# Kernel tuning notes

Hardware: AMD Instinct MI355X
Metric: run time of the kernel (lower is better)

Reference implementation:

```python
import jax, jax.numpy as jnp
import numpy as np

N = 100000   # nodes
E = 1600000  # edges (avg degree 16)
D = 128      # in_dim


def setup_inputs() -> dict:
    key = jax.random.key(0)
    k = jax.random.split(key, 8)
    h = jax.random.normal(k[0], (N, D), dtype=jnp.float32)
    d = jax.random.uniform(k[1], (N,), dtype=jnp.float32)  # per-node degree norm (e.g. deg^-0.5)
    yes_no = jax.random.uniform(k[2], (E,), dtype=jnp.float32)
    gate_w = jax.random.normal(k[3], (1, 2 * D), dtype=jnp.float32) * (1.414 / np.sqrt(2 * D))
    gate_b = jnp.zeros((1,), dtype=jnp.float32)
    yes_weight = jax.random.uniform(k[4], (), dtype=jnp.float32)
    no_weight = jax.random.uniform(k[5], (), dtype=jnp.float32)
    src = jax.random.randint(k[6], (E,), 0, N, dtype=jnp.int64)
    dst = jax.random.randint(k[7], (E,), 0, N, dtype=jnp.int64)
    return {"h": h, "d": d, "yes_no": yes_no, "gate_w": gate_w, "gate_b": gate_b,
            "yes_weight": yes_weight, "no_weight": no_weight, "src": src, "dst": dst}


def reference(h, d, yes_no, gate_w, gate_b, yes_weight, no_weight, src, dst):
    n, dim = h.shape
    # gate(cat[h_dst, h_src]) == h_dst @ W[:, :D].T + h_src @ W[:, D:].T + b
    # project once per node, then gather per edge (avoids [E, 2D] concat)
    p_dst = h @ gate_w[0, :dim]  # [N]
    p_src = h @ gate_w[0, dim:]  # [N]
    g = jnp.tanh(p_dst[dst] + p_src[src] + gate_b[0])  # [E]
    yn = jnp.tanh(yes_no * yes_weight + (1.0 - yes_no) * no_weight)  # [E]
    e = (g + yn) * 0.5 * d[dst] * d[src]  # [E] (dropout p=0 -> identity)
    m = h[src] * e[:, None]  # [E, D] edge messages
    z = jax.ops.segment_sum(m, dst, num_segments=n)  # [N, D]
    return z
```

## Files before the change

kernel.cpp:

```cpp
#include <hip/hip_runtime.h>

#define D 128
#define NPB 250
#define NBMAX 512
#define EPB 2048
#define BCAP 5120

typedef unsigned short u16x8 __attribute__((ext_vector_type(8)));
typedef float          f32x8 __attribute__((ext_vector_type(8)));
typedef float          f32x4 __attribute__((ext_vector_type(4)));

__device__ __forceinline__ unsigned short f2bf(float x) {
    unsigned int u = __float_as_uint(x);
    u += 0x7FFFu + ((u >> 16) & 1u);
    return (unsigned short)(u >> 16);
}
__device__ __forceinline__ float bf2f(unsigned short b) {
    return __uint_as_float(((unsigned int)b) << 16);
}
__device__ __forceinline__ float fast_tanh(float x) {
    float e = __expf(2.0f * x);
    return 1.0f - 2.0f * __builtin_amdgcn_rcpf(e + 1.0f);
}

__global__ __launch_bounds__(256) void proj_kernel(const float* __restrict__ h,
                                                   const float* __restrict__ gw,
                                                   const float* __restrict__ dnorm,
                                                   float4* __restrict__ q,
                                                   unsigned short* __restrict__ hb,
                                                   unsigned int* __restrict__ tails,
                                                   int n_nodes) {
    if (blockIdx.x == 0) {
        tails[threadIdx.x] = 0u;
        tails[threadIdx.x + 256] = 0u;
    }
    int node = (int)((blockIdx.x * blockDim.x + threadIdx.x) >> 6);
    int lane = threadIdx.x & 63;
    if (node >= n_nodes) return;
    const float2* hr2 = (const float2*)(h + (size_t)node * D);
    const float2* gw2 = (const float2*)gw;
    float2 hv = hr2[lane];
    float2 wa = gw2[lane];
    float2 wb = gw2[lane + 64];
    ushort2 hvb = make_ushort2(f2bf(hv.x), f2bf(hv.y));
    *(ushort2*)(hb + (size_t)node * D + 2 * lane) = hvb;
    float s1 = hv.x * wa.x + hv.y * wa.y;
    float s2 = hv.x * wb.x + hv.y * wb.y;
    #pragma unroll
    for (int off = 32; off > 0; off >>= 1) {
        s1 += __shfl_down(s1, off, 64);
        s2 += __shfl_down(s2, off, 64);
    }
    if (lane == 0) q[node] = make_float4(s1, s2, dnorm[node], 0.0f);
}

__global__ __launch_bounds__(512) void bin_kernel(const float4* __restrict__ q,
                                                  const float* __restrict__ yes_no,
                                                  const int* __restrict__ src,
                                                  const int* __restrict__ dst,
                                                  const float* __restrict__ gate_b,
                                                  const float* __restrict__ yes_w,
                                                  const float* __restrict__ no_w,
                                                  unsigned int* __restrict__ tails,
                                                  unsigned long long* __restrict__ recs,
                                                  int n_edges, int nb) {
    __shared__ unsigned long long sorted[EPB];
    __shared__ unsigned int hist[NBMAX];
    __shared__ unsigned int sbuf[NBMAX];
    __shared__ unsigned int base[NBMAX];
    __shared__ unsigned int cursor[NBMAX];
    __shared__ unsigned int gbase[NBMAX];

    int tid = threadIdx.x;
    int e0 = blockIdx.x * EPB;
    int n = n_edges - e0;
    if (n > EPB) n = EPB;

    hist[tid] = 0u;
    __syncthreads();

    for (int j = tid; j < n; j += 512) {
        unsigned int d = (unsigned int)dst[e0 + j];
        atomicAdd(&hist[d / NPB], 1u);
    }
    __syncthreads();

    sbuf[tid] = hist[tid];
    __syncthreads();
    unsigned int* pa = sbuf;
    unsigned int* pb = gbase;
    #pragma unroll
    for (int s = 1; s < NBMAX; s <<= 1) {
        unsigned int v = pa[tid] + ((tid >= s) ? pa[tid - s] : 0u);
        pb[tid] = v;
        __syncthreads();
        unsigned int* t = pa; pa = pb; pb = t;
    }
    unsigned int ex = (tid == 0) ? 0u : pa[tid - 1];
    base[tid] = ex;
    cursor[tid] = ex;
    __syncthreads();

    float gb = gate_b[0];
    float yw = yes_w[0];
    float nw = no_w[0];

    for (int j = tid; j < n; j += 512) {
        int e = e0 + j;
        int dd = dst[e];
        int ss = src[e];
        float yn = yes_no[e];
        float4 qt = q[dd];
        float4 qs = q[ss];
        float g = fast_tanh(qt.x + qs.y + gb);
        float y = fast_tanh(yn * yw + (1.0f - yn) * nw);
        float ce = (g + y) * 0.5f * qt.z * qs.z;
        int qv = (int)rintf(ce * 8191.0f) + 8192;
        unsigned int w0 = ((unsigned int)ss << 15) | (unsigned int)qv;
        unsigned int bk = (unsigned int)dd / NPB;
        unsigned int pos = atomicAdd(&cursor[bk], 1u);
        sorted[pos] = ((unsigned long long)(unsigned int)dd << 32) | (unsigned long long)w0;
    }
    __syncthreads();

    gbase[tid] = (hist[tid] > 0u) ? atomicAdd(&tails[tid], hist[tid]) : 0u;
    __syncthreads();

    for (int j = tid; j < n; j += 512) {
        unsigned long long r = sorted[j];
        unsigned int bk = (unsigned int)(r >> 32) / NPB;
        unsigned int gpos = gbase[bk] + ((unsigned int)j - base[bk]);
        if (gpos < BCAP)
            __builtin_nontemporal_store(r, recs + (size_t)bk * BCAP + gpos);
    }
}

__global__ __launch_bounds__(512) void gscat_kernel(const unsigned int* __restrict__ tails,
                                                    const unsigned long long* __restrict__ recs,
                                                    const unsigned short* __restrict__ hb,
                                                    float* __restrict__ z,
                                                    int n_nodes) {
    __shared__ unsigned int sw0[BCAP];
    __shared__ unsigned int hist2[256];
    __shared__ unsigned int sa[256];
    __shared__ unsigned int sb[256];
    __shared__ unsigned int rowbase[256];
    __shared__ unsigned int cursor2[256];

    int b = blockIdx.x;
    int tid = threadIdx.x;
    unsigned int nrec = tails[b];
    if (nrec > BCAP) nrec = BCAP;
    const unsigned long long* rb = recs + (size_t)b * BCAP;
    int node0 = b * NPB;

    if (tid < 256) hist2[tid] = 0u;
    __syncthreads();

    for (unsigned int j = tid; j < nrec; j += 512) {
        unsigned long long r = rb[j];
        unsigned int nl = (unsigned int)(r >> 32) - (unsigned int)node0;
        atomicAdd(&hist2[nl], 1u);
    }
    __syncthreads();

    if (tid < 256) sa[tid] = hist2[tid];
    __syncthreads();
    unsigned int* pa = sa;
    unsigned int* pb = sb;
    #pragma unroll
    for (int s = 1; s < 256; s <<= 1) {
        if (tid < 256) {
            unsigned int v = pa[tid] + ((tid >= s) ? pa[tid - s] : 0u);
            pb[tid] = v;
        }
        __syncthreads();
        unsigned int* t = pa; pa = pb; pb = t;
    }
    if (tid < 256) {
        unsigned int ex = (tid == 0) ? 0u : pa[tid - 1];
        rowbase[tid] = ex;
        cursor2[tid] = ex;
    }
    __syncthreads();

    for (unsigned int j = tid; j < nrec; j += 512) {
        unsigned long long r = rb[j];
        unsigned int nl = (unsigned int)(r >> 32) - (unsigned int)node0;
        unsigned int pos = atomicAdd(&cursor2[nl], 1u);
        sw0[pos] = (unsigned int)r;
    }
    __syncthreads();

    int grp  = tid >> 4;
    int lane = tid & 15;
    const unsigned short* hbl = hb + 8 * lane;
    const float inv = 1.0f / 8191.0f;
    for (int nl = grp; nl < NPB; nl += 32) {
        int node = node0 + nl;
        if (node >= n_nodes) break;
        unsigned int base2 = rowbase[nl];
        int n = (int)hist2[nl];
        f32x8 acc = (f32x8)0.0f;
        int k = 0;
        for (; k + 3 < n; k += 4) {
            unsigned int e0 = sw0[base2 + k],     e1 = sw0[base2 + k + 1];
            unsigned int e2 = sw0[base2 + k + 2], e3 = sw0[base2 + k + 3];
            float c0 = (float)((int)(e0 & 0x7fffu) - 8192) * inv;
            float c1 = (float)((int)(e1 & 0x7fffu) - 8192) * inv;
            float c2 = (float)((int)(e2 & 0x7fffu) - 8192) * inv;
            float c3 = (float)((int)(e3 & 0x7fffu) - 8192) * inv;
            u16x8 a = *(const u16x8*)(hbl + (size_t)(e0 >> 15) * D);
            u16x8 bb = *(const u16x8*)(hbl + (size_t)(e1 >> 15) * D);
            u16x8 c = *(const u16x8*)(hbl + (size_t)(e2 >> 15) * D);
            u16x8 d = *(const u16x8*)(hbl + (size_t)(e3 >> 15) * D);
            #pragma unroll
            for (int j = 0; j < 8; ++j) {
                acc[j] += bf2f(a[j]) * c0 + bf2f(bb[j]) * c1 + bf2f(c[j]) * c2 + bf2f(d[j]) * c3;
            }
        }
        for (; k < n; ++k) {
            unsigned int e0 = sw0[base2 + k];
            float c0 = (float)((int)(e0 & 0x7fffu) - 8192) * inv;
            u16x8 a = *(const u16x8*)(hbl + (size_t)(e0 >> 15) * D);
            #pragma unroll
            for (int j = 0; j < 8; ++j) acc[j] += bf2f(a[j]) * c0;
        }
        f32x4 lo = { acc[0], acc[1], acc[2], acc[3] };
        f32x4 hi = { acc[4], acc[5], acc[6], acc[7] };
        f32x4* zp = (f32x4*)(z + (size_t)node * D + 8 * lane);
        __builtin_nontemporal_store(lo, zp);
        __builtin_nontemporal_store(hi, zp + 1);
    }
}

extern "C" void kernel_launch(void* const* d_in, const int* in_sizes, int n_in,
                              void* d_out, int out_size, void* d_ws, size_t ws_size,
                              hipStream_t stream) {
    const float* h       = (const float*)d_in[0];
    const float* dnorm   = (const float*)d_in[1];
    const float* yes_no  = (const float*)d_in[2];
    const float* gate_w  = (const float*)d_in[3];
    const float* gate_b  = (const float*)d_in[4];
    const float* yes_w   = (const float*)d_in[5];
    const float* no_w    = (const float*)d_in[6];
    const int*   src     = (const int*)d_in[7];
    const int*   dst     = (const int*)d_in[8];

    int n_nodes = in_sizes[0] / D;
    int n_edges = in_sizes[2];
    int nb = (n_nodes + NPB - 1) / NPB;

    char* ws = (char*)d_ws;
    size_t off = 0;
    auto take = [&](size_t bytes) {
        void* ptr = ws + off;
        off += (bytes + 15) & ~(size_t)15;
        return ptr;
    };
    float4*             q     = (float4*)take((size_t)n_nodes * sizeof(float4));
    unsigned short*     hb    = (unsigned short*)take((size_t)n_nodes * D * sizeof(unsigned short));
    unsigned int*       tails = (unsigned int*)take((size_t)NBMAX * sizeof(unsigned int));
    unsigned long long* recs  = (unsigned long long*)take((size_t)nb * BCAP * sizeof(unsigned long long));
    (void)ws_size;

    proj_kernel<<<(n_nodes + 3) / 4, 256, 0, stream>>>(h, gate_w, dnorm, q, hb, tails, n_nodes);

    bin_kernel<<<(n_edges + EPB - 1) / EPB, 512, 0, stream>>>(
        q, yes_no, src, dst, gate_b, yes_w, no_w, tails, recs, n_edges, nb);

    gscat_kernel<<<nb, 512, 0, stream>>>(tails, recs, hb, (float*)d_out, n_nodes);
}
```

Baseline: 238.3 us.

## Enlarge node buckets, pad per-block bucket segments to 8-record alignment

Raises nodes per bucket from 250 to 391, which reduces the bucket count to about 256 and gives larger scatter blocks. Each bin block now rounds its per-bucket reservation up to a multiple of 8 records and fills the padding with sentinel records, so global writes land on aligned 64-byte runs. The gather kernel widens its scan to 512 entries and skips the sentinels. The cost is padding traffic, a larger LDS record buffer that may lower occupancy, and truncation if a bucket overflows the shared capacity.

Result: slower. 257.7 us (+8.1%).

```diff
diff --git a/kernel.cpp b/kernel.cpp
--- a/kernel.cpp
+++ b/kernel.cpp
@@ -1,10 +1,11 @@
 #include <hip/hip_runtime.h>
 
 #define D 128
-#define NPB 250
+#define NPB 391
 #define NBMAX 512
 #define EPB 2048
-#define BCAP 5120
+#define BCAP 10240
+#define BCAPS 7168
 
 typedef unsigned short u16x8 __attribute__((ext_vector_type(8)));
 typedef float          f32x8 __attribute__((ext_vector_type(8)));
@@ -123,7 +124,11 @@
     }
     __syncthreads();
 
-    gbase[tid] = (hist[tid] > 0u) ? atomicAdd(&tails[tid], hist[tid]) : 0u;
+    {
+        unsigned int c  = hist[tid];
+        unsigned int ru = (c + 7u) & ~7u;
+        gbase[tid] = ru ? atomicAdd(&tails[tid], ru) : 0u;
+    }
     __syncthreads();
 
     for (int j = tid; j < n; j += 512) {
@@ -133,6 +138,16 @@
         if (gpos < BCAP)
             __builtin_nontemporal_store(r, recs + (size_t)bk * BCAP + gpos);
     }
+    {
+        unsigned int c  = hist[tid];
+        unsigned int ru = (c + 7u) & ~7u;
+        for (unsigned int p = c; p < ru; ++p) {
+            unsigned int gpos = gbase[tid] + p;
+            if (gpos < BCAP)
+                __builtin_nontemporal_store(0xFFFFFFFF00000000ULL,
+                                            recs + (size_t)tid * BCAP + gpos);
+        }
+    }
 }
 
 __global__ __launch_bounds__(512) void gscat_kernel(const unsigned int* __restrict__ tails,
@@ -140,12 +155,12 @@
                                                     const unsigned short* __restrict__ hb,
                                                     float* __restrict__ z,
                                                     int n_nodes) {
-    __shared__ unsigned int sw0[BCAP];
-    __shared__ unsigned int hist2[256];
-    __shared__ unsigned int sa[256];
-    __shared__ unsigned int sb[256];
-    __shared__ unsigned int rowbase[256];
-    __shared__ unsigned int cursor2[256];
+    __shared__ unsigned int sw0[BCAPS];
+    __shared__ unsigned int hist2[NBMAX];
+    __shared__ unsigned int sa[NBMAX];
+    __shared__ unsigned int sb[NBMAX];
+    __shared__ unsigned int rowbase[NBMAX];
+    __shared__ unsigned int cursor2[NBMAX];
 
     int b = blockIdx.x;
     int tid = threadIdx.x;
@@ -154,41 +169,39 @@
     const unsigned long long* rb = recs + (size_t)b * BCAP;
     int node0 = b * NPB;
 
-    if (tid < 256) hist2[tid] = 0u;
+    hist2[tid] = 0u;
     __syncthreads();
 
     for (unsigned int j = tid; j < nrec; j += 512) {
         unsigned long long r = rb[j];
         unsigned int nl = (unsigned int)(r >> 32) - (unsigned int)node0;
-        atomicAdd(&hist2[nl], 1u);
-    }
-    __syncthreads();
-
-    if (tid < 256) sa[tid] = hist2[tid];
+        if (nl < (unsigned int)NPB) atomicAdd(&hist2[nl], 1u);
+    }
+    __syncthreads();
+
+    sa[tid] = hist2[tid];
     __syncthreads();
     unsigned int* pa = sa;
     unsigned int* pb = sb;
     #pragma unroll
-    for (int s = 1; s < 256; s <<= 1) {
-        if (tid < 256) {
-            unsigned int v = pa[tid] + ((tid >= s) ? pa[tid - s] : 0u);
-            pb[tid] = v;
-        }
+    for (int s = 1; s < NBMAX; s <<= 1) {
+        unsigned int v = pa[tid] + ((tid >= s) ? pa[tid - s] : 0u);
+        pb[tid] = v;
         __syncthreads();
         unsigned int* t = pa; pa = pb; pb = t;
     }
-    if (tid < 256) {
-        unsigned int ex = (tid == 0) ? 0u : pa[tid - 1];
-        rowbase[tid] = ex;
-        cursor2[tid] = ex;
-    }
+    unsigned int ex = (tid == 0) ? 0u : pa[tid - 1];
+    rowbase[tid] = ex;
+    cursor2[tid] = ex;
     __syncthreads();
 
     for (unsigned int j = tid; j < nrec; j += 512) {
         unsigned long long r = rb[j];
         unsigned int nl = (unsigned int)(r >> 32) - (unsigned int)node0;
-        unsigned int pos = atomicAdd(&cursor2[nl], 1u);
-        sw0[pos] = (unsigned int)r;
+        if (nl < (unsigned int)NPB) {
+            unsigned int pos = atomicAdd(&cursor2[nl], 1u);
+            if (pos < BCAPS) sw0[pos] = (unsigned int)r;
+        }
     }
     __syncthreads();
 
@@ -201,6 +214,8 @@
         if (node >= n_nodes) break;
         unsigned int base2 = rowbase[nl];
         int n = (int)hist2[nl];
+        if (base2 >= BCAPS) n = 0;
+        else if (n > (int)(BCAPS - base2)) n = (int)(BCAPS - base2);
         f32x8 acc = (f32x8)0.0f;
         int k = 0;
         for (; k + 3 < n; k += 4) {
@@ -255,7 +270,7 @@
     size_t off = 0;
     auto take = [&](size_t bytes) {
         void* ptr = ws + off;
-        off += (bytes + 15) & ~(size_t)15;
+        off += (bytes + 63) & ~(size_t)63;
         return ptr;
     };
     float4*             q     = (float4*)take((size_t)n_nodes * sizeof(float4));
```

## Replace global bucket atomics with per-block sorted chunks and an offset directory

Applied to the files above, without the earlier changes.

The binning kernel now writes each block's locally bucket-sorted edge records contiguously, plus a 16-bit directory of per-bucket start offsets, instead of reserving space in global per-bucket arrays through atomics and scattering records there. The gather/scatter kernel then has each thread read one source block's segment for its node bucket through that directory. Edges per binning block grow from 2048 to 4096 so the number of source blocks fits in one 512-thread block. This removes the global atomic tail counters, their zeroing, and the scattered second pass. In exchange, each thread now walks its segment serially and uncoalesced, and LDS use in the binning kernel grows.

After: 248.4 us. 1.04x slower.

```diff
diff --git a/kernel.cpp b/kernel.cpp
--- a/kernel.cpp
+++ b/kernel.cpp
@@ -3,8 +3,8 @@
 #define D 128
 #define NPB 250
 #define NBMAX 512
-#define EPB 2048
-#define BCAP 5120
+#define EPB 4096
+#define BCAPS 5120
 
 typedef unsigned short u16x8 __attribute__((ext_vector_type(8)));
 typedef float          f32x8 __attribute__((ext_vector_type(8)));
@@ -28,12 +28,7 @@
                                                    const float* __restrict__ dnorm,
                                                    float4* __restrict__ q,
                                                    unsigned short* __restrict__ hb,
-                                                   unsigned int* __restrict__ tails,
                                                    int n_nodes) {
-    if (blockIdx.x == 0) {
-        tails[threadIdx.x] = 0u;
-        tails[threadIdx.x + 256] = 0u;
-    }
     int node = (int)((blockIdx.x * blockDim.x + threadIdx.x) >> 6);
     int lane = threadIdx.x & 63;
     if (node >= n_nodes) return;
@@ -61,15 +56,15 @@
                                                   const float* __restrict__ gate_b,
                                                   const float* __restrict__ yes_w,
                                                   const float* __restrict__ no_w,
-                                                  unsigned int* __restrict__ tails,
                                                   unsigned long long* __restrict__ recs,
-                                                  int n_edges, int nb) {
+                                                  unsigned short* __restrict__ dir16,
+                                                  int n_edges) {
     __shared__ unsigned long long sorted[EPB];
     __shared__ unsigned int hist[NBMAX];
     __shared__ unsigned int sbuf[NBMAX];
+    __shared__ unsigned int scr[NBMAX];
     __shared__ unsigned int base[NBMAX];
     __shared__ unsigned int cursor[NBMAX];
-    __shared__ unsigned int gbase[NBMAX];
 
     int tid = threadIdx.x;
     int e0 = blockIdx.x * EPB;
@@ -88,7 +83,7 @@
     sbuf[tid] = hist[tid];
     __syncthreads();
     unsigned int* pa = sbuf;
-    unsigned int* pb = gbase;
+    unsigned int* pb = scr;
     #pragma unroll
     for (int s = 1; s < NBMAX; s <<= 1) {
         unsigned int v = pa[tid] + ((tid >= s) ? pa[tid - s] : 0u);
@@ -123,24 +118,18 @@
     }
     __syncthreads();
 
-    gbase[tid] = (hist[tid] > 0u) ? atomicAdd(&tails[tid], hist[tid]) : 0u;
-    __syncthreads();
-
-    for (int j = tid; j < n; j += 512) {
-        unsigned long long r = sorted[j];
-        unsigned int bk = (unsigned int)(r >> 32) / NPB;
-        unsigned int gpos = gbase[bk] + ((unsigned int)j - base[bk]);
-        if (gpos < BCAP)
-            __builtin_nontemporal_store(r, recs + (size_t)bk * BCAP + gpos);
-    }
-}
-
-__global__ __launch_bounds__(512) void gscat_kernel(const unsigned int* __restrict__ tails,
-                                                    const unsigned long long* __restrict__ recs,
+    unsigned long long* out = recs + (size_t)blockIdx.x * EPB;
+    for (int j = tid; j < n; j += 512)
+        __builtin_nontemporal_store(sorted[j], out + j);
+    dir16[(size_t)blockIdx.x * NBMAX + tid] = (unsigned short)base[tid];
+}
+
+__global__ __launch_bounds__(512) void gscat_kernel(const unsigned long long* __restrict__ recs,
+                                                    const unsigned short* __restrict__ dir16,
                                                     const unsigned short* __restrict__ hb,
                                                     float* __restrict__ z,
-                                                    int n_nodes) {
-    __shared__ unsigned int sw0[BCAP];
+                                                    int n_nodes, int nsb) {
+    __shared__ unsigned int sw0[BCAPS];
     __shared__ unsigned int hist2[256];
     __shared__ unsigned int sa[256];
     __shared__ unsigned int sb[256];
@@ -149,18 +138,24 @@
 
     int b = blockIdx.x;
     int tid = threadIdx.x;
-    unsigned int nrec = tails[b];
-    if (nrec > BCAP) nrec = BCAP;
-    const unsigned long long* rb = recs + (size_t)b * BCAP;
     int node0 = b * NPB;
 
     if (tid < 256) hist2[tid] = 0u;
     __syncthreads();
 
-    for (unsigned int j = tid; j < nrec; j += 512) {
-        unsigned long long r = rb[j];
-        unsigned int nl = (unsigned int)(r >> 32) - (unsigned int)node0;
-        atomicAdd(&hist2[nl], 1u);
+    unsigned int off0 = 0u, cnt0 = 0u;
+    if (tid < nsb) {
+        const unsigned short* dr = dir16 + (size_t)tid * NBMAX + b;
+        unsigned int a0 = dr[0];
+        unsigned int a1 = dr[1];
+        off0 = a0;
+        cnt0 = a1 - a0;
+    }
+    const unsigned long long* seg = recs + (size_t)tid * EPB + off0;
+
+    for (unsigned int r = 0; r < cnt0; ++r) {
+        unsigned int nl = (unsigned int)(seg[r] >> 32) - (unsigned int)node0;
+        if (nl < (unsigned int)NPB) atomicAdd(&hist2[nl], 1u);
     }
     __syncthreads();
 
@@ -184,11 +179,13 @@
     }
     __syncthreads();
 
-    for (unsigned int j = tid; j < nrec; j += 512) {
-        unsigned long long r = rb[j];
-        unsigned int nl = (unsigned int)(r >> 32) - (unsigned int)node0;
-        unsigned int pos = atomicAdd(&cursor2[nl], 1u);
-        sw0[pos] = (unsigned int)r;
+    for (unsigned int r = 0; r < cnt0; ++r) {
+        unsigned long long rec = seg[r];
+        unsigned int nl = (unsigned int)(rec >> 32) - (unsigned int)node0;
+        if (nl < (unsigned int)NPB) {
+            unsigned int pos = atomicAdd(&cursor2[nl], 1u);
+            if (pos < BCAPS) sw0[pos] = (unsigned int)rec;
+        }
     }
     __syncthreads();
 
@@ -201,6 +198,8 @@
         if (node >= n_nodes) break;
         unsigned int base2 = rowbase[nl];
         int n = (int)hist2[nl];
+        if (base2 >= BCAPS) n = 0;
+        else if (n > (int)(BCAPS - base2)) n = (int)(BCAPS - base2);
         f32x8 acc = (f32x8)0.0f;
         int k = 0;
         for (; k + 3 < n; k += 4) {
@@ -249,25 +248,26 @@
 
     int n_nodes = in_sizes[0] / D;
     int n_edges = in_sizes[2];
-    int nb = (n_nodes + NPB - 1) / NPB;
+    int nb  = (n_nodes + NPB - 1) / NPB;
+    int nsb = (n_edges + EPB - 1) / EPB;
 
     char* ws = (char*)d_ws;
     size_t off = 0;
     auto take = [&](size_t bytes) {
         void* ptr = ws + off;
-        off += (bytes + 15) & ~(size_t)15;
+        off += (bytes + 63) & ~(size_t)63;
         return ptr;
     };
     float4*             q     = (float4*)take((size_t)n_nodes * sizeof(float4));
     unsigned short*     hb    = (unsigned short*)take((size_t)n_nodes * D * sizeof(unsigned short));
-    unsigned int*       tails = (unsigned int*)take((size_t)NBMAX * sizeof(unsigned int));
-    unsigned long long* recs  = (unsigned long long*)take((size_t)nb * BCAP * sizeof(unsigned long long));
+    unsigned long long* recs  = (unsigned long long*)take((size_t)nsb * EPB * sizeof(unsigned long long));
+    unsigned short*     dir16 = (unsigned short*)take((size_t)nsb * NBMAX * sizeof(unsigned short));
     (void)ws_size;
 
-    proj_kernel<<<(n_nodes + 3) / 4, 256, 0, stream>>>(h, gate_w, dnorm, q, hb, tails, n_nodes);
-
-    bin_kernel<<<(n_edges + EPB - 1) / EPB, 512, 0, stream>>>(
-        q, yes_no, src, dst, gate_b, yes_w, no_w, tails, recs, n_edges, nb);
-
-    gscat_kernel<<<nb, 512, 0, stream>>>(tails, recs, hb, (float*)d_out, n_nodes);
-}
+    proj_kernel<<<(n_nodes + 3) / 4, 256, 0, stream>>>(h, gate_w, dnorm, q, hb, n_nodes);
+
+    bin_kernel<<<nsb, 512, 0, stream>>>(
+        q, yes_no, src, dst, gate_b, yes_w, no_w, recs, dir16, n_edges);
+
+    gscat_kernel<<<nb, 512, 0, stream>>>(recs, dir16, hb, (float*)d_out, n_nodes, nsb);
+}
```
